# Kernel tuning notes

Hardware: AMD Instinct MI355X
Metric: run time of the kernel (lower is better)

## Reference

```python
import jax, jax.numpy as jnp
import numpy as np

N, E, MUL, ATTR, NBASIS = 30000, 480000, 32, 8, 8
AVG_NEIGH = 16.0
INV_SQRT3 = 1.0 / np.sqrt(3.0).astype(np.float32)  # wigner 3j (1,1,0)
LOG2 = float(np.log(2.0))


def ssp(x):
    # shifted softplus: softplus(x) - log(2)
    return jax.nn.softplus(x) - LOG2


def setup_inputs() -> dict:
    key = jax.random.key(0)
    ks = jax.random.split(key, 15)
    return {
        "node_s": jax.random.normal(ks[0], (N, MUL), jnp.float32),
        "node_v": jax.random.normal(ks[1], (N, MUL, 3), jnp.float32),
        "node_attr": jax.random.uniform(ks[2], (N, ATTR), jnp.float32),
        "edge_attr": jax.random.normal(ks[3], (E, 4), jnp.float32),       # [sh0 | sh1(3)]
        "edge_scalars": jax.random.uniform(ks[4], (E, NBASIS), jnp.float32),
        "W1_0": jax.random.normal(ks[5], (MUL, MUL), jnp.float32),
        "W1_1": jax.random.normal(ks[6], (MUL, MUL), jnp.float32),
        "Wfc1": jax.random.normal(ks[7], (NBASIS, NBASIS), jnp.float32),
        "Wfc2": jax.random.normal(ks[8], (NBASIS, 4 * MUL), jnp.float32),
        "W2_0": jax.random.normal(ks[9], (2 * MUL, MUL), jnp.float32),
        "W2_1": jax.random.normal(ks[10], (2 * MUL, MUL), jnp.float32),
        "Wsc0": jax.random.normal(ks[11], (MUL, ATTR, MUL), jnp.float32),
        "Wsc1": jax.random.normal(ks[12], (MUL, ATTR, MUL), jnp.float32),
        "edge_src": jax.random.randint(ks[13], (E,), 0, N, jnp.int32),
        "edge_dst": jax.random.randint(ks[14], (E,), 0, N, jnp.int32),
    }


def reference(node_s, node_v, node_attr, edge_attr, edge_scalars,
              W1_0, W1_1, Wfc1, Wfc2, W2_0, W2_1, Wsc0, Wsc1,
              edge_src, edge_dst):
    n_nodes, mul = node_s.shape
    # --- fc: radial MLP -> per-edge TP weights (shared_weights=False) ---
    h = ssp(edge_scalars @ Wfc1 * (1.0 / np.sqrt(Wfc1.shape[0])))
    w = h @ Wfc2 * (1.0 / np.sqrt(Wfc2.shape[0]))                 # [E, 4*MUL]
    w00, w01, w10, w11 = jnp.split(w, 4, axis=1)                  # instruction order
    # --- lin1: per-irrep linear (fan-in normalized) ---
    inv_m = 1.0 / np.sqrt(mul)
    x0 = node_s @ W1_0 * inv_m                                    # [N, MUL]
    x1 = jnp.einsum('nud,uw->nwd', node_v, W1_1) * inv_m          # [N, MUL, 3]
    # --- gather destination-node features per edge ---
    x0d, x1d = x0[edge_dst], x1[edge_dst]
    sh0, sh1 = edge_attr[:, :1], edge_attr[:, 1:4]
    # --- uvu tensor product with per-edge weights ---
    s_a = w00 * x0d * sh0                                         # 0e x 0e -> 0e
    s_b = w11 * jnp.einsum('eud,ed->eu', x1d, sh1) * INV_SQRT3    # 1o x 1o -> 0e
    v_a = (w01 * x0d)[:, :, None] * sh1[:, None, :]               # 0e x 1o -> 1o
    v_b = w10[:, :, None] * x1d * sh0[:, :, None]                 # 1o x 0e -> 1o
    mid_s = jnp.concatenate([s_a, s_b], axis=1)                   # [E, 64]  (64x0e)
    mid_v = jnp.concatenate([v_a, v_b], axis=1)                   # [E, 64, 3] (64x1o)
    # --- scatter-sum over edge_src, normalized by sqrt(avg_num_neighbors) ---
    inv_nb = 1.0 / np.sqrt(AVG_NEIGH)
    agg_s = jax.ops.segment_sum(mid_s, edge_src, num_segments=n_nodes) * inv_nb
    agg_v = jax.ops.segment_sum(mid_v, edge_src, num_segments=n_nodes) * inv_nb
    # --- lin2 ---
    inv_2m = 1.0 / np.sqrt(2.0 * mul)
    out0 = agg_s @ W2_0 * inv_2m                                  # [N, MUL]
    out1 = jnp.einsum('nud,uw->nwd', agg_v, W2_1) * inv_2m        # [N, MUL, 3]
    # --- self-connection: fully-connected TP (attr is scalar 8x0e) ---
    sc_norm = 1.0 / np.sqrt(mul * node_attr.shape[1])
    sc0 = jnp.einsum('nu,nv,uvw->nw', node_s, node_attr, Wsc0) * sc_norm
    sc1 = jnp.einsum('nud,nv,uvw->nwd', node_v, node_attr, Wsc1) * sc_norm
    o0 = out0 + sc0
    o1 = out1 + sc1
    return jnp.concatenate([o0, o1.reshape(n_nodes, mul * 3)], axis=1)  # [N, 128]
```

## Files before the change

### kernel.cpp

```cpp
#include <hip/hip_runtime.h>
#include <math.h>

#define N_NODES 30000
#define N_EDGES 480000

typedef __attribute__((ext_vector_type(8))) short short8;
typedef __attribute__((ext_vector_type(4))) float f32x4;

__device__ __forceinline__ unsigned short f2bf(float f) {
    unsigned u = __float_as_uint(f);
    u += 0x7fff + ((u >> 16) & 1);
    return (unsigned short)(u >> 16);
}
__device__ __forceinline__ float bfLO(unsigned v) { return __uint_as_float(v << 16); }
__device__ __forceinline__ float bfHI(unsigned v) { return __uint_as_float(v & 0xffff0000u); }
__device__ __forceinline__ unsigned packbf(float a, float b) {
    return (unsigned)f2bf(a) | ((unsigned)f2bf(b) << 16);
}
__device__ __forceinline__ unsigned ptk(float a, float b) {
    return (__float_as_uint(a) >> 16) | (__float_as_uint(b) & 0xffff0000u);
}

union U8 { short8 v; unsigned u[4]; };
union C4 { f32x4 v; float f[4]; };

__global__ __launch_bounds__(256) void k_pre(
    const float* __restrict__ node_s,
    const float* __restrict__ node_v,
    const float* __restrict__ W1_0,
    const float* __restrict__ W1_1,
    const float* __restrict__ Wsc0,
    const float* __restrict__ Wsc1,
    const float* __restrict__ W2_0,
    const float* __restrict__ W2_1,
    const int* __restrict__ edge_src,
    int* __restrict__ deg,
    unsigned short* __restrict__ xnode,
    unsigned* __restrict__ bsc0,
    unsigned* __restrict__ bsc1,
    unsigned* __restrict__ b20,
    unsigned* __restrict__ b21)
{
    __shared__ float sW0[1024];
    __shared__ float sW1[1024];
    int tid = threadIdx.x;

    if (blockIdx.x >= 3750) {
        int b = blockIdx.x - 3750;
        const float* Wm = (b == 0) ? Wsc0 : (b == 1) ? Wsc1 : (b == 2) ? W2_0 : W2_1;
        unsigned* dst = (b == 0) ? bsc0 : (b == 1) ? bsc1 : (b == 2) ? b20 : b21;
        float scale = (b < 2) ? 0.0625f : 0.03125f;
        int nu = (b < 2) ? 4096 : 1024;
        for (int idx = tid; idx < nu; idx += 256) {
            int jp = idx & 3;
            int lane = (idx >> 2) & 63;
            int ft = (idx >> 8) & 1;
            int kc = idx >> 9;
            int quad = lane >> 4, col = lane & 15;
            int k = kc * 32 + quad * 8 + jp * 2;
            int c = ft * 16 + col;
            dst[idx] = packbf(Wm[k * 32 + c] * scale, Wm[(k + 1) * 32 + c] * scale);
        }
        return;
    }

    if (tid < 128) atomicAdd(&deg[edge_src[blockIdx.x * 128 + tid]], 1);
    for (int i = tid; i < 1024; i += 256) { sW0[i] = W1_0[i]; sW1[i] = W1_1[i]; }
    __syncthreads();
    int node = blockIdx.x * 8 + (tid >> 5);
    int w = tid & 31;
    const float inv_m = 0.1767766953f;
    float x0 = 0.f, x1a = 0.f, x1b = 0.f, x1c = 0.f;
    const float* sp = node_s + (size_t)node * 32;
    const float* vp = node_v + (size_t)node * 96;
#pragma unroll
    for (int u = 0; u < 32; ++u) {
        float su = sp[u];
        float w0 = sW0[u * 32 + w];
        float w1 = sW1[u * 32 + w];
        x0 = fmaf(su, w0, x0);
        x1a = fmaf(vp[u * 3 + 0], w1, x1a);
        x1b = fmaf(vp[u * 3 + 1], w1, x1b);
        x1c = fmaf(vp[u * 3 + 2], w1, x1c);
    }
    uint2 pk;
    pk.x = packbf(x0 * inv_m, x1a * inv_m);
    pk.y = packbf(x1b * inv_m, x1c * inv_m);
    *(uint2*)(xnode + (size_t)node * 128 + w * 4) = pk;
}

__global__ __launch_bounds__(1024) void scan_kernel(const int* __restrict__ deg,
                                                    int* __restrict__ offs,
                                                    int* __restrict__ cursor) {
    __shared__ int sdeg[N_NODES];
    __shared__ int wsum[16];
    int tid = threadIdx.x;
#pragma unroll
    for (int k = 0; k < 30; ++k) {
        int idx = k * 1024 + tid;
        if (idx < N_NODES) sdeg[idx] = deg[idx];
    }
    __syncthreads();
    int base = tid * 30;
    int s = 0;
    if (base < N_NODES) {
#pragma unroll
        for (int k = 0; k < 30; ++k) s += sdeg[base + k];
    }
    int lane = tid & 63, wid = tid >> 6;
    int inc = s;
#pragma unroll
    for (int d = 1; d < 64; d <<= 1) {
        int o = __shfl_up(inc, d, 64);
        if (lane >= d) inc += o;
    }
    if (lane == 63) wsum[wid] = inc;
    __syncthreads();
    if (tid < 16) {
        int v = wsum[tid];
        int t = v;
#pragma unroll
        for (int d = 1; d < 16; d <<= 1) {
            int o = __shfl_up(t, d, 64);
            if (tid >= d) t += o;
        }
        wsum[tid] = t - v;
    }
    __syncthreads();
    int run = inc - s + wsum[wid];
    if (base < N_NODES) {
#pragma unroll
        for (int k = 0; k < 30; ++k) {
            int n = base + k;
            int d = sdeg[n];
            sdeg[n] = run;
            run += d;
        }
    }
    __syncthreads();
#pragma unroll
    for (int k = 0; k < 30; ++k) {
        int idx = k * 1024 + tid;
        if (idx < N_NODES) {
            int v = sdeg[idx];
            offs[idx] = v;
            cursor[idx] = v;
        }
    }
    if (tid == 0) offs[N_NODES] = N_EDGES;
}

__global__ __launch_bounds__(256) void fill_kernel(
    const float* __restrict__ edge_attr,
    const float* __restrict__ edge_scalars,
    const float* __restrict__ Wfc1,
    const int* __restrict__ edge_src,
    const int* __restrict__ edge_dst,
    int* __restrict__ cursor,
    unsigned short* __restrict__ hE,
    unsigned short* __restrict__ eaE,
    int2* __restrict__ edPerm)
{
    __shared__ float sW[64];
    int tid = threadIdx.x;
    if (tid < 64) sW[tid] = Wfc1[tid];
    __syncthreads();

    int e = blockIdx.x * 256 + tid;
    float4 es0 = *(const float4*)(edge_scalars + (size_t)e * 8);
    float4 es1 = *(const float4*)(edge_scalars + (size_t)e * 8 + 4);
    float4 ea  = *(const float4*)(edge_attr + (size_t)e * 4);
    int src = edge_src[e];
    int dst = edge_dst[e];
    int pos = atomicAdd(&cursor[src], 1);

    const float inv8 = 0.3535533906f;
    float h[8];
#pragma unroll
    for (int i = 0; i < 8; ++i) {
        float acc = es0.x * sW[0 * 8 + i];
        acc = fmaf(es0.y, sW[1 * 8 + i], acc);
        acc = fmaf(es0.z, sW[2 * 8 + i], acc);
        acc = fmaf(es0.w, sW[3 * 8 + i], acc);
        acc = fmaf(es1.x, sW[4 * 8 + i], acc);
        acc = fmaf(es1.y, sW[5 * 8 + i], acc);
        acc = fmaf(es1.z, sW[6 * 8 + i], acc);
        acc = fmaf(es1.w, sW[7 * 8 + i], acc);
        acc *= inv8;
        float ax = fabsf(acc);
        float tt = __expf(-ax);
        h[i] = fmaxf(acc, 0.f) + __logf(1.f + tt) - 0.6931471806f;
    }
    uint4 hp;
    hp.x = packbf(h[0], h[1]); hp.y = packbf(h[2], h[3]);
    hp.z = packbf(h[4], h[5]); hp.w = packbf(h[6], h[7]);
    *(uint4*)(hE + (size_t)e * 8) = hp;
    uint2 eo;
    eo.x = packbf(ea.x, ea.y); eo.y = packbf(ea.z, ea.w);
    *(uint2*)(eaE + (size_t)e * 4) = eo;
    int2 ed; ed.x = dst; ed.y = e;
    edPerm[pos] = ed;
}

__global__ __launch_bounds__(256) void gather_kernel(
    const int* __restrict__ offs,
    const int2* __restrict__ edPerm,
    const unsigned short* __restrict__ hE,
    const unsigned short* __restrict__ eaE,
    const float* __restrict__ Wfc2,
    const unsigned short* __restrict__ xnode,
    unsigned short* __restrict__ agg)
{
    int tid = threadIdx.x;
    int lane = tid & 63;
    int u = lane & 31;
    int half = lane >> 5;
    int node = blockIdx.x * 4 + (tid >> 6);

    const float inv8 = 0.3535533906f;
    const float inv_s3 = 0.5773502692f;
    float wf0[8], wf1[8], wf2[8], wf3[8];
#pragma unroll
    for (int i = 0; i < 8; ++i) {
        wf0[i] = Wfc2[i * 128 + u] * inv8;
        wf1[i] = Wfc2[i * 128 + 32 + u] * inv8;
        wf2[i] = Wfc2[i * 128 + 64 + u] * inv8;
        wf3[i] = Wfc2[i * 128 + 96 + u] * inv8 * inv_s3;
    }

    int beg = offs[node], end = offs[node + 1];
    float a_sa = 0.f, a_sb = 0.f;
    float a_va0 = 0.f, a_va1 = 0.f, a_va2 = 0.f;
    float a_vb0 = 0.f, a_vb1 = 0.f, a_vb2 = 0.f;

    if (end > beg) {
        int last = end - 1;
        int i = beg + half;
        int2 edA = edPerm[min(i, last)];
        int2 edB = edPerm[min(i + 2, last)];
        int2 edC = edPerm[min(i + 4, last)];
        uint2 xA = *(const uint2*)(xnode + (size_t)edA.x * 128 + u * 4);
        uint4 hA = *(const uint4*)(hE + (size_t)edA.y * 8);
        uint2 eA = *(const uint2*)(eaE + (size_t)edA.y * 4);
        uint2 xB = *(const uint2*)(xnode + (size_t)edB.x * 128 + u * 4);
        uint4 hB = *(const uint4*)(hE + (size_t)edB.y * 8);
        uint2 eB = *(const uint2*)(eaE + (size_t)edB.y * 4);

        for (; i < end; i += 2) {
            int2 edD = edPerm[min(i + 6, last)];
            uint2 xC = *(const uint2*)(xnode + (size_t)edC.x * 128 + u * 4);
            uint4 hC = *(const uint4*)(hE + (size_t)edC.y * 8);
            uint2 eC = *(const uint2*)(eaE + (size_t)edC.y * 4);

            float h0 = bfLO(hA.x), h1 = bfHI(hA.x), h2 = bfLO(hA.y), h3 = bfHI(hA.y);
            float h4 = bfLO(hA.z), h5 = bfHI(hA.z), h6 = bfLO(hA.w), h7 = bfHI(hA.w);
            float a00 = h0 * wf0[0], a01 = h0 * wf1[0], a10 = h0 * wf2[0], a11 = h0 * wf3[0];
            a00 = fmaf(h1, wf0[1], a00); a01 = fmaf(h1, wf1[1], a01); a10 = fmaf(h1, wf2[1], a10); a11 = fmaf(h1, wf3[1], a11);
            a00 = fmaf(h2, wf0[2], a00); a01 = fmaf(h2, wf1[2], a01); a10 = fmaf(h2, wf2[2], a10); a11 = fmaf(h2, wf3[2], a11);
            a00 = fmaf(h3, wf0[3], a00); a01 = fmaf(h3, wf1[3], a01); a10 = fmaf(h3, wf2[3], a10); a11 = fmaf(h3, wf3[3], a11);
            a00 = fmaf(h4, wf0[4], a00); a01 = fmaf(h4, wf1[4], a01); a10 = fmaf(h4, wf2[4], a10); a11 = fmaf(h4, wf3[4], a11);
            a00 = fmaf(h5, wf0[5], a00); a01 = fmaf(h5, wf1[5], a01); a10 = fmaf(h5, wf2[5], a10); a11 = fmaf(h5, wf3[5], a11);
            a00 = fmaf(h6, wf0[6], a00); a01 = fmaf(h6, wf1[6], a01); a10 = fmaf(h6, wf2[6], a10); a11 = fmaf(h6, wf3[6], a11);
            a00 = fmaf(h7, wf0[7], a00); a01 = fmaf(h7, wf1[7], a01); a10 = fmaf(h7, wf2[7], a10); a11 = fmaf(h7, wf3[7], a11);

            float sh0 = bfLO(eA.x), s1xe = bfHI(eA.x), s1ye = bfLO(eA.y), s1ze = bfHI(eA.y);
            float x0 = bfLO(xA.x), xd0 = bfHI(xA.x), xd1 = bfLO(xA.y), xd2 = bfHI(xA.y);

            float dot = xd0 * s1xe + xd1 * s1ye + xd2 * s1ze;
            a_sa = fmaf(a00 * sh0, x0, a_sa);
            a_sb = fmaf(a11, dot, a_sb);
            float w01x0 = a01 * x0;
            a_va0 = fmaf(w01x0, s1xe, a_va0);
            a_va1 = fmaf(w01x0, s1ye, a_va1);
            a_va2 = fmaf(w01x0, s1ze, a_va2);
            float t10 = a10 * sh0;
            a_vb0 = fmaf(t10, xd0, a_vb0);
            a_vb1 = fmaf(t10, xd1, a_vb1);
            a_vb2 = fmaf(t10, xd2, a_vb2);

            hA = hB; eA = eB; xA = xB;
            hB = hC; eB = eC; xB = xC;
            edC = edD;
        }
    }
    a_sa  += __shfl_xor(a_sa, 32, 64);
    a_sb  += __shfl_xor(a_sb, 32, 64);
    a_va0 += __shfl_xor(a_va0, 32, 64);
    a_va1 += __shfl_xor(a_va1, 32, 64);
    a_va2 += __shfl_xor(a_va2, 32, 64);
    a_vb0 += __shfl_xor(a_vb0, 32, 64);
    a_vb1 += __shfl_xor(a_vb1, 32, 64);
    a_vb2 += __shfl_xor(a_vb2, 32, 64);

    unsigned short* ap = agg + (size_t)node * 256;
    if (half == 0) {
        ap[u]       = f2bf(a_sa);
        ap[32 + u]  = f2bf(a_sb);
        ap[64 + u]  = f2bf(a_va0);
        ap[96 + u]  = f2bf(a_vb0);
    } else {
        ap[128 + u] = f2bf(a_va1);
        ap[160 + u] = f2bf(a_vb1);
        ap[192 + u] = f2bf(a_va2);
        ap[224 + u] = f2bf(a_vb2);
    }
}

__global__ __launch_bounds__(256) void k_post(
    const float* __restrict__ node_s,
    const float* __restrict__ node_v,
    const float* __restrict__ node_attr,
    const unsigned* __restrict__ bsc0,
    const unsigned* __restrict__ bsc1,
    const unsigned* __restrict__ b20,
    const unsigned* __restrict__ b21,
    const unsigned short* __restrict__ agg,
    float* __restrict__ out)
{
    __shared__ float stg[4][688];
    int tid = threadIdx.x;
    int lane = tid & 63;
    int wv = tid >> 6;
    int t = blockIdx.x * 4 + wv;
    int col = lane & 15;
    int quad = lane >> 4;
    int m = lane & 15;
    bool is_s = (t < 1875);

    const short* Bs = (const short*)(is_s ? bsc0 : bsc1);
    const short* B2 = (const short*)(is_s ? b20 : b21);
    short8 bs0[8], bs1[8], b2f[2][2];
#pragma unroll
    for (int kc = 0; kc < 8; ++kc) {
        bs0[kc] = *(const short8*)(Bs + ((kc * 2 + 0) * 64 + lane) * 8);
        bs1[kc] = *(const short8*)(Bs + ((kc * 2 + 1) * 64 + lane) * 8);
    }
#pragma unroll
    for (int kc = 0; kc < 2; ++kc) {
#pragma unroll
        for (int ft = 0; ft < 2; ++ft)
            b2f[kc][ft] = *(const short8*)(B2 + ((kc * 2 + ft) * 64 + lane) * 8);
    }

    float* S = stg[wv];
    int fbase, fstep, n_a, aoff;
    if (is_s) {
        for (int q = lane; q < 512; q += 64)
            S[(q >> 5) * 33 + (q & 31)] = node_s[(size_t)t * 512 + q];
        n_a = t * 16 + m;
        fbase = m * 33;
        fstep = 1;
        aoff = n_a * 256;
    } else {
        int vt = t - 1875;
        int R0 = vt * 16;
        int nlo = R0 / 3;
        int nhi = (R0 + 15) / 3;
        int cnt = (nhi - nlo + 1) * 96;
        const float* src = node_v + (size_t)nlo * 96;
        for (int q = lane; q < cnt; q += 64)
            S[(q / 96) * 97 + (q % 96)] = src[q];
        int R = R0 + m;
        n_a = R / 3;
        int d_a = R - n_a * 3;
        fbase = (n_a - nlo) * 97 + d_a;
        fstep = 3;
        aoff = n_a * 256 + 64 + 64 * d_a;
    }
    float4 A0 = *(const float4*)(node_attr + (size_t)n_a * 8);
    float4 A1 = *(const float4*)(node_attr + (size_t)n_a * 8 + 4);
    float aa0 = A0.x, aa1 = A0.y, aa2 = A0.z, aa3 = A0.w;
    float aa4 = A1.x, aa5 = A1.y, aa6 = A1.z, aa7 = A1.w;

    f32x4 acc0 = {0.f, 0.f, 0.f, 0.f};
    f32x4 acc1 = {0.f, 0.f, 0.f, 0.f};

#pragma unroll
    for (int kc = 0; kc < 2; ++kc) {
        short8 af = *(const short8*)((const short*)agg + (size_t)aoff + kc * 32 + quad * 8);
        acc0 = __builtin_amdgcn_mfma_f32_16x16x32_bf16(af, b2f[kc][0], acc0, 0, 0, 0);
        acc1 = __builtin_amdgcn_mfma_f32_16x16x32_bf16(af, b2f[kc][1], acc1, 0, 0, 0);
    }

#pragma unroll
    for (int kc = 0; kc < 8; ++kc) {
        int u = kc * 4 + quad;
        float f = S[fbase + u * fstep];
        U8 af;
        af.u[0] = ptk(f * aa0, f * aa1);
        af.u[1] = ptk(f * aa2, f * aa3);
        af.u[2] = ptk(f * aa4, f * aa5);
        af.u[3] = ptk(f * aa6, f * aa7);
        acc0 = __builtin_amdgcn_mfma_f32_16x16x32_bf16(af.v, bs0[kc], acc0, 0, 0, 0);
        acc1 = __builtin_amdgcn_mfma_f32_16x16x32_bf16(af.v, bs1[kc], acc1, 0, 0, 0);
    }

    C4 c0, c1;
    c0.v = acc0; c1.v = acc1;
    if (is_s) {
#pragma unroll
        for (int r = 0; r < 4; ++r) {
            int n = t * 16 + (quad << 2) + r;
            out[(size_t)n * 128 + col]      = c0.f[r];
            out[(size_t)n * 128 + col + 16] = c1.f[r];
        }
    } else {
        int R0 = (t - 1875) * 16;
#pragma unroll
        for (int r = 0; r < 4; ++r) {
            int R = R0 + (quad << 2) + r;
            int nn = R / 3;
            int dd = R - nn * 3;
            out[(size_t)nn * 128 + 32 + 3 * col + dd]        = c0.f[r];
            out[(size_t)nn * 128 + 32 + 3 * (col + 16) + dd] = c1.f[r];
        }
    }
}

extern "C" void kernel_launch(void* const* d_in, const int* in_sizes, int n_in,
                              void* d_out, int out_size, void* d_ws, size_t ws_size,
                              hipStream_t stream) {
    const float* node_s       = (const float*)d_in[0];
    const float* node_v       = (const float*)d_in[1];
    const float* node_attr    = (const float*)d_in[2];
    const float* edge_attr    = (const float*)d_in[3];
    const float* edge_scalars = (const float*)d_in[4];
    const float* W1_0 = (const float*)d_in[5];
    const float* W1_1 = (const float*)d_in[6];
    const float* Wfc1 = (const float*)d_in[7];
    const float* Wfc2 = (const float*)d_in[8];
    const float* W2_0 = (const float*)d_in[9];
    const float* W2_1 = (const float*)d_in[10];
    const float* Wsc0 = (const float*)d_in[11];
    const float* Wsc1 = (const float*)d_in[12];
    const int* edge_src = (const int*)d_in[13];
    const int* edge_dst = (const int*)d_in[14];

    char* ws = (char*)d_ws;
    unsigned short* xnode = (unsigned short*)(ws);
    unsigned short* hE    = (unsigned short*)(ws + 7680000);
    unsigned short* eaE   = (unsigned short*)(ws + 15360000);
    int2* edPerm          = (int2*)(ws + 19200000);
    unsigned short* agg   = (unsigned short*)(ws + 23040000);
    int* deg    = (int*)(ws + 38400000);
    int* offs   = (int*)(ws + 38520000);
    int* cursor = (int*)(ws + 38640016);
    unsigned* bsc0 = (unsigned*)(ws + 38760064);
    unsigned* bsc1 = (unsigned*)(ws + 38776448);
    unsigned* b20  = (unsigned*)(ws + 38792832);
    unsigned* b21  = (unsigned*)(ws + 38796928);

    hipMemsetAsync(deg, 0, (size_t)N_NODES * sizeof(int), stream);
    k_pre<<<3754, 256, 0, stream>>>(node_s, node_v, W1_0, W1_1, Wsc0, Wsc1,
                                    W2_0, W2_1, edge_src, deg, xnode,
                                    bsc0, bsc1, b20, b21);
    scan_kernel<<<1, 1024, 0, stream>>>(deg, offs, cursor);
    fill_kernel<<<1875, 256, 0, stream>>>(edge_attr, edge_scalars, Wfc1,
                                          edge_src, edge_dst, cursor, hE, eaE, edPerm);
    gather_kernel<<<7500, 256, 0, stream>>>(offs, edPerm, hE, eaE, Wfc2, xnode, agg);
    k_post<<<1875, 256, 0, stream>>>(node_s, node_v, node_attr,
                                     bsc0, bsc1, b20, b21, agg, (float*)d_out);
}
```

Before: 242.6 us.

## Pack per-edge data into sorted 32-byte records and batch two nodes per thread in pre-pass

```diff
diff --git a/kernel.cpp b/kernel.cpp
--- a/kernel.cpp
+++ b/kernel.cpp
@@ -23,6 +23,8 @@
 
 union U8 { short8 v; unsigned u[4]; };
 union C4 { f32x4 v; float f[4]; };
+
+#define VE(A, B, C, idx) ((idx) < 4 ? (&(A).x)[(idx)] : (idx) < 8 ? (&(B).x)[(idx) - 4] : (&(C).x)[(idx) - 8])
 
 __global__ __launch_bounds__(256) void k_pre(
     const float* __restrict__ node_s,
@@ -41,12 +43,11 @@
     unsigned* __restrict__ b20,
     unsigned* __restrict__ b21)
 {
-    __shared__ float sW0[1024];
-    __shared__ float sW1[1024];
+    __shared__ unsigned sW1p[1024];
     int tid = threadIdx.x;
 
-    if (blockIdx.x >= 3750) {
-        int b = blockIdx.x - 3750;
+    if (blockIdx.x >= 1875) {
+        int b = blockIdx.x - 1875;
         const float* Wm = (b == 0) ? Wsc0 : (b == 1) ? Wsc1 : (b == 2) ? W2_0 : W2_1;
         unsigned* dst = (b == 0) ? bsc0 : (b == 1) ? bsc1 : (b == 2) ? b20 : b21;
         float scale = (b < 2) ? 0.0625f : 0.03125f;
@@ -64,29 +65,51 @@
         return;
     }
 
-    if (tid < 128) atomicAdd(&deg[edge_src[blockIdx.x * 128 + tid]], 1);
-    for (int i = tid; i < 1024; i += 256) { sW0[i] = W1_0[i]; sW1[i] = W1_1[i]; }
-    __syncthreads();
-    int node = blockIdx.x * 8 + (tid >> 5);
+    atomicAdd(&deg[edge_src[blockIdx.x * 256 + tid]], 1);
+    for (int i = tid; i < 1024; i += 256) sW1p[i] = packbf(W1_0[i], W1_1[i]);
+    __syncthreads();
+
     int w = tid & 31;
+    int n0 = blockIdx.x * 16 + (tid >> 5) * 2;
     const float inv_m = 0.1767766953f;
-    float x0 = 0.f, x1a = 0.f, x1b = 0.f, x1c = 0.f;
-    const float* sp = node_s + (size_t)node * 32;
-    const float* vp = node_v + (size_t)node * 96;
-#pragma unroll
-    for (int u = 0; u < 32; ++u) {
-        float su = sp[u];
-        float w0 = sW0[u * 32 + w];
-        float w1 = sW1[u * 32 + w];
-        x0 = fmaf(su, w0, x0);
-        x1a = fmaf(vp[u * 3 + 0], w1, x1a);
-        x1b = fmaf(vp[u * 3 + 1], w1, x1b);
-        x1c = fmaf(vp[u * 3 + 2], w1, x1c);
-    }
-    uint2 pk;
-    pk.x = packbf(x0 * inv_m, x1a * inv_m);
-    pk.y = packbf(x1b * inv_m, x1c * inv_m);
-    *(uint2*)(xnode + (size_t)node * 128 + w * 4) = pk;
+    float x0[2] = {0.f, 0.f}, x1a[2] = {0.f, 0.f};
+    float x1b[2] = {0.f, 0.f}, x1c[2] = {0.f, 0.f};
+
+    for (int uc = 0; uc < 32; uc += 4) {
+        float4 sv[2], v0[2], v1[2], v2[2];
+#pragma unroll
+        for (int j = 0; j < 2; ++j) {
+            sv[j] = *(const float4*)(node_s + (size_t)(n0 + j) * 32 + uc);
+            const float* vp = node_v + (size_t)(n0 + j) * 96 + uc * 3;
+            v0[j] = *(const float4*)(vp);
+            v1[j] = *(const float4*)(vp + 4);
+            v2[j] = *(const float4*)(vp + 8);
+        }
+#pragma unroll
+        for (int kk = 0; kk < 4; ++kk) {
+            int u = uc + kk;
+            unsigned wp = sW1p[u * 32 + w];
+            float w0k = bfLO(wp), w1k = bfHI(wp);
+#pragma unroll
+            for (int j = 0; j < 2; ++j) {
+                float s  = (&sv[j].x)[kk];
+                float vx = VE(v0[j], v1[j], v2[j], kk * 3 + 0);
+                float vy = VE(v0[j], v1[j], v2[j], kk * 3 + 1);
+                float vz = VE(v0[j], v1[j], v2[j], kk * 3 + 2);
+                x0[j]  = fmaf(s,  w0k, x0[j]);
+                x1a[j] = fmaf(vx, w1k, x1a[j]);
+                x1b[j] = fmaf(vy, w1k, x1b[j]);
+                x1c[j] = fmaf(vz, w1k, x1c[j]);
+            }
+        }
+    }
+#pragma unroll
+    for (int j = 0; j < 2; ++j) {
+        uint2 pk;
+        pk.x = packbf(x0[j] * inv_m, x1a[j] * inv_m);
+        pk.y = packbf(x1b[j] * inv_m, x1c[j] * inv_m);
+        *(uint2*)(xnode + (size_t)(n0 + j) * 128 + w * 4) = pk;
+    }
 }
 
 __global__ __launch_bounds__(1024) void scan_kernel(const int* __restrict__ deg,
@@ -157,9 +180,7 @@
     const int* __restrict__ edge_src,
     const int* __restrict__ edge_dst,
     int* __restrict__ cursor,
-    unsigned short* __restrict__ hE,
-    unsigned short* __restrict__ eaE,
-    int2* __restrict__ edPerm)
+    uint4* __restrict__ rec)
 {
     __shared__ float sW[64];
     int tid = threadIdx.x;
@@ -191,22 +212,18 @@
         float tt = __expf(-ax);
         h[i] = fmaxf(acc, 0.f) + __logf(1.f + tt) - 0.6931471806f;
     }
-    uint4 hp;
-    hp.x = packbf(h[0], h[1]); hp.y = packbf(h[2], h[3]);
-    hp.z = packbf(h[4], h[5]); hp.w = packbf(h[6], h[7]);
-    *(uint4*)(hE + (size_t)e * 8) = hp;
-    uint2 eo;
-    eo.x = packbf(ea.x, ea.y); eo.y = packbf(ea.z, ea.w);
-    *(uint2*)(eaE + (size_t)e * 4) = eo;
-    int2 ed; ed.x = dst; ed.y = e;
-    edPerm[pos] = ed;
+    uint4 r0, r1;
+    r0.x = packbf(h[0], h[1]); r0.y = packbf(h[2], h[3]);
+    r0.z = packbf(h[4], h[5]); r0.w = packbf(h[6], h[7]);
+    r1.x = packbf(ea.x, ea.y); r1.y = packbf(ea.z, ea.w);
+    r1.z = (unsigned)dst; r1.w = 0;
+    rec[2 * pos]     = r0;
+    rec[2 * pos + 1] = r1;
 }
 
 __global__ __launch_bounds__(256) void gather_kernel(
     const int* __restrict__ offs,
-    const int2* __restrict__ edPerm,
-    const unsigned short* __restrict__ hE,
-    const unsigned short* __restrict__ eaE,
+    const uint4* __restrict__ rec,
     const float* __restrict__ Wfc2,
     const unsigned short* __restrict__ xnode,
     unsigned short* __restrict__ agg)
@@ -236,24 +253,22 @@
     if (end > beg) {
         int last = end - 1;
         int i = beg + half;
-        int2 edA = edPerm[min(i, last)];
-        int2 edB = edPerm[min(i + 2, last)];
-        int2 edC = edPerm[min(i + 4, last)];
-        uint2 xA = *(const uint2*)(xnode + (size_t)edA.x * 128 + u * 4);
-        uint4 hA = *(const uint4*)(hE + (size_t)edA.y * 8);
-        uint2 eA = *(const uint2*)(eaE + (size_t)edA.y * 4);
-        uint2 xB = *(const uint2*)(xnode + (size_t)edB.x * 128 + u * 4);
-        uint4 hB = *(const uint4*)(hE + (size_t)edB.y * 8);
-        uint2 eB = *(const uint2*)(eaE + (size_t)edB.y * 4);
+        int p = min(i, last);
+        uint4 a0 = rec[2 * p], a1 = rec[2 * p + 1];
+        p = min(i + 2, last);
+        uint4 b0 = rec[2 * p], b1 = rec[2 * p + 1];
+        p = min(i + 4, last);
+        uint4 c0 = rec[2 * p], c1 = rec[2 * p + 1];
+        uint2 xA = *(const uint2*)(xnode + (size_t)(int)a1.z * 128 + u * 4);
+        uint2 xB = *(const uint2*)(xnode + (size_t)(int)b1.z * 128 + u * 4);
 
         for (; i < end; i += 2) {
-            int2 edD = edPerm[min(i + 6, last)];
-            uint2 xC = *(const uint2*)(xnode + (size_t)edC.x * 128 + u * 4);
-            uint4 hC = *(const uint4*)(hE + (size_t)edC.y * 8);
-            uint2 eC = *(const uint2*)(eaE + (size_t)edC.y * 4);
-
-            float h0 = bfLO(hA.x), h1 = bfHI(hA.x), h2 = bfLO(hA.y), h3 = bfHI(hA.y);
-            float h4 = bfLO(hA.z), h5 = bfHI(hA.z), h6 = bfLO(hA.w), h7 = bfHI(hA.w);
+            int pD = min(i + 6, last);
+            uint4 d0 = rec[2 * pD], d1 = rec[2 * pD + 1];
+            uint2 xC = *(const uint2*)(xnode + (size_t)(int)c1.z * 128 + u * 4);
+
+            float h0 = bfLO(a0.x), h1 = bfHI(a0.x), h2 = bfLO(a0.y), h3 = bfHI(a0.y);
+            float h4 = bfLO(a0.z), h5 = bfHI(a0.z), h6 = bfLO(a0.w), h7 = bfHI(a0.w);
             float a00 = h0 * wf0[0], a01 = h0 * wf1[0], a10 = h0 * wf2[0], a11 = h0 * wf3[0];
             a00 = fmaf(h1, wf0[1], a00); a01 = fmaf(h1, wf1[1], a01); a10 = fmaf(h1, wf2[1], a10); a11 = fmaf(h1, wf3[1], a11);
             a00 = fmaf(h2, wf0[2], a00); a01 = fmaf(h2, wf1[2], a01); a10 = fmaf(h2, wf2[2], a10); a11 = fmaf(h2, wf3[2], a11);
@@ -263,7 +278,7 @@
             a00 = fmaf(h6, wf0[6], a00); a01 = fmaf(h6, wf1[6], a01); a10 = fmaf(h6, wf2[6], a10); a11 = fmaf(h6, wf3[6], a11);
             a00 = fmaf(h7, wf0[7], a00); a01 = fmaf(h7, wf1[7], a01); a10 = fmaf(h7, wf2[7], a10); a11 = fmaf(h7, wf3[7], a11);
 
-            float sh0 = bfLO(eA.x), s1xe = bfHI(eA.x), s1ye = bfLO(eA.y), s1ze = bfHI(eA.y);
+            float sh0 = bfLO(a1.x), s1xe = bfHI(a1.x), s1ye = bfLO(a1.y), s1ze = bfHI(a1.y);
             float x0 = bfLO(xA.x), xd0 = bfHI(xA.x), xd1 = bfLO(xA.y), xd2 = bfHI(xA.y);
 
             float dot = xd0 * s1xe + xd1 * s1ye + xd2 * s1ze;
@@ -278,9 +293,9 @@
             a_vb1 = fmaf(t10, xd1, a_vb1);
             a_vb2 = fmaf(t10, xd2, a_vb2);
 
-            hA = hB; eA = eB; xA = xB;
-            hB = hC; eB = eC; xB = xC;
-            edC = edD;
+            a0 = b0; a1 = b1; xA = xB;
+            b0 = c0; b1 = c1; xB = xC;
+            c0 = d0; c1 = d1;
         }
     }
     a_sa  += __shfl_xor(a_sa, 32, 64);
@@ -381,7 +396,6 @@
         acc0 = __builtin_amdgcn_mfma_f32_16x16x32_bf16(af, b2f[kc][0], acc0, 0, 0, 0);
         acc1 = __builtin_amdgcn_mfma_f32_16x16x32_bf16(af, b2f[kc][1], acc1, 0, 0, 0);
     }
-
 #pragma unroll
     for (int kc = 0; kc < 8; ++kc) {
         int u = kc * 4 + quad;
@@ -438,9 +452,7 @@
 
     char* ws = (char*)d_ws;
     unsigned short* xnode = (unsigned short*)(ws);
-    unsigned short* hE    = (unsigned short*)(ws + 7680000);
-    unsigned short* eaE   = (unsigned short*)(ws + 15360000);
-    int2* edPerm          = (int2*)(ws + 19200000);
+    uint4* rec            = (uint4*)(ws + 7680000);
     unsigned short* agg   = (unsigned short*)(ws + 23040000);
     int* deg    = (int*)(ws + 38400000);
     int* offs   = (int*)(ws + 38520000);
@@ -451,13 +463,13 @@
     unsigned* b21  = (unsigned*)(ws + 38796928);
 
     hipMemsetAsync(deg, 0, (size_t)N_NODES * sizeof(int), stream);
-    k_pre<<<3754, 256, 0, stream>>>(node_s, node_v, W1_0, W1_1, Wsc0, Wsc1,
+    k_pre<<<1879, 256, 0, stream>>>(node_s, node_v, W1_0, W1_1, Wsc0, Wsc1,
                                     W2_0, W2_1, edge_src, deg, xnode,
                                     bsc0, bsc1, b20, b21);
     scan_kernel<<<1, 1024, 0, stream>>>(deg, offs, cursor);
     fill_kernel<<<1875, 256, 0, stream>>>(edge_attr, edge_scalars, Wfc1,
-                                          edge_src, edge_dst, cursor, hE, eaE, edPerm);
-    gather_kernel<<<7500, 256, 0, stream>>>(offs, edPerm, hE, eaE, Wfc2, xnode, agg);
+                                          edge_src, edge_dst, cursor, rec);
+    gather_kernel<<<7500, 256, 0, stream>>>(offs, rec, Wfc2, xnode, agg);
     k_post<<<1875, 256, 0, stream>>>(node_s, node_v, node_attr,
                                      bsc0, bsc1, b20, b21, agg, (float*)d_out);
 }
```

After: 240.8 us. No clear change (-0.8%).
